# Optimization experiments

Measured on AMD Instinct MI355X. Metric: run time of the kernel, lower is better.

Reference implementation:

```python
import jax, jax.numpy as jnp
import numpy as np

N = 4096
F_IN = 256
F_OUT = 64
H = 4
ALPHA = 0.2  # leaky_relu negative slope
NEG_BIG = -9e15


def setup_inputs() -> dict:
    key = jax.random.key(0)
    k1, k2, k3, k4 = jax.random.split(key, 4)
    x = jax.random.normal(k1, (N, F_IN), dtype=jnp.float32)
    adj = jax.random.randint(k2, (N, N), 0, 2, dtype=jnp.int32)
    # xavier-uniform-like init for params
    limW = float(np.sqrt(6.0 / (F_IN + F_OUT)))
    W = jax.random.uniform(k3, (H, F_IN, F_OUT), jnp.float32, -limW, limW)
    lima = float(np.sqrt(6.0 / (2 * F_OUT + 1)))
    a = jax.random.uniform(k4, (H, 2 * F_OUT, 1), jnp.float32, -lima, lima)
    return {"x": x, "adj": adj, "W": W, "a": a}


def reference(x, adj, W, a):
    # Wh[h,n,o] = x @ W[h]
    Wh = jnp.einsum('nf,hfo->hno', x, W)
    # split attention vector: e[h,i,j] = leaky_relu(a1.Wh_i + a2.Wh_j)
    a1 = a[:, :F_OUT, 0]   # [H, F_OUT]
    a2 = a[:, F_OUT:, 0]   # [H, F_OUT]
    s1 = jnp.einsum('hno,ho->hn', Wh, a1)  # [H, N]
    s2 = jnp.einsum('hno,ho->hn', Wh, a2)  # [H, N]
    e = jax.nn.leaky_relu(s1[:, :, None] + s2[:, None, :], ALPHA)  # [H, N, N]
    e = jnp.where(adj[None, :, :] > 0, e, NEG_BIG)
    att = jax.nn.softmax(e, axis=-1)
    # dropout=0 (eval-mode reference)
    h_prime = jnp.einsum('hij,hjo->hio', att, Wh)  # [H, N, F_OUT]
    # concat heads -> [N, H*F_OUT]
    return jnp.transpose(h_prime, (1, 0, 2)).reshape(N, H * F_OUT)
```

## Files before the change

### kernel.cpp

```cpp
#include <hip/hip_runtime.h>

#define NN 4096
#define FIN 256
#define FOUT 64
#define NH 4

using f32x4 = __attribute__((ext_vector_type(4))) float;
using s16x8 = __attribute__((ext_vector_type(8))) short;
typedef unsigned long long u64;

__device__ __forceinline__ unsigned short f32_to_bf16_rne(float f) {
    unsigned b = __float_as_uint(f);
    b += 0x7FFFu + ((b >> 16) & 1u);
    return (unsigned short)(b >> 16);
}
__device__ __forceinline__ unsigned encf(float f) {
    unsigned b = __float_as_uint(f);
    return (b & 0x80000000u) ? ~b : (b | 0x80000000u);
}
__device__ __forceinline__ float decf(unsigned u) {
    return (u & 0x80000000u) ? __uint_as_float(u & 0x7FFFFFFFu) : __uint_as_float(~u);
}

__global__ __launch_bounds__(256) void k_wh(
    const float* __restrict__ x, const float* __restrict__ W,
    const float* __restrict__ a, short* __restrict__ WhT,
    float* __restrict__ s1, float* __restrict__ s2, unsigned* __restrict__ s2m)
{
    __shared__ unsigned short xs[64 * 256];
    __shared__ unsigned short wt[64 * 256];
    __shared__ float s2red[16];
    const int nb = blockIdx.x, h = blockIdx.y, t = threadIdx.x;
    const int n0 = nb * 64;
    {
        const float4* xg = reinterpret_cast<const float4*>(x + (size_t)n0 * FIN);
        for (int k = t; k < 64 * FIN / 4; k += 256) {
            float4 v = xg[k];
            int row = k >> 6, fq = k & 63;
            u64 pk = (u64)f32_to_bf16_rne(v.x) | ((u64)f32_to_bf16_rne(v.y) << 16)
                   | ((u64)f32_to_bf16_rne(v.z) << 32) | ((u64)f32_to_bf16_rne(v.w) << 48);
            int byte = (row * 512 + fq * 8) ^ ((row & 7) << 4);
            *(u64*)((char*)xs + byte) = pk;
        }
        const float* Wg = W + (size_t)h * FIN * FOUT;
        for (int k = t; k < FIN * FOUT; k += 256) {
            int f = k >> 6, o = k & 63;
            unsigned short wv = f32_to_bf16_rne(Wg[k]);
            int byte = (o * 512 + f * 2) ^ ((o & 7) << 4);
            *(unsigned short*)((char*)wt + byte) = wv;
        }
    }
    __syncthreads();
    const int lane = t & 63, wv_ = t >> 6;
    const int rowA = lane & 15;
    const int kq = (lane >> 4) * 8;
    const int i0 = wv_ * 16;
    f32x4 acc[4];
    #pragma unroll
    for (int c = 0; c < 4; ++c) acc[c] = (f32x4){0.f, 0.f, 0.f, 0.f};
    const int arow = i0 + rowA;
    #pragma unroll
    for (int kb = 0; kb < FIN; kb += 32) {
        int ab = (arow * 512 + (kb + kq) * 2) ^ ((arow & 7) << 4);
        s16x8 af = *(const s16x8*)((char*)xs + ab);
        #pragma unroll
        for (int c = 0; c < 4; ++c) {
            int col = c * 16 + rowA;
            int bb = (col * 512 + (kb + kq) * 2) ^ ((col & 7) << 4);
            s16x8 bf = *(const s16x8*)((char*)wt + bb);
            acc[c] = __builtin_amdgcn_mfma_f32_16x16x32_bf16(af, bf, acc[c], 0, 0, 0);
        }
    }
    const int q0 = (lane >> 4) * 4;
    const float L2E = 1.4426950408889634f;
    float v1acc[4] = {0.f, 0.f, 0.f, 0.f}, v2acc[4] = {0.f, 0.f, 0.f, 0.f};
    #pragma unroll
    for (int c = 0; c < 4; ++c) {
        int col = c * 16 + rowA;
        float a1v = a[h * (2 * FOUT) + col];
        float a2v = a[h * (2 * FOUT) + FOUT + col];
        short* wp = WhT + ((size_t)(h * FOUT + col)) * NN + n0 + i0 + q0;
        alignas(8) unsigned short tmp[4];
        #pragma unroll
        for (int q = 0; q < 4; ++q) {
            float v = acc[c][q];
            tmp[q] = f32_to_bf16_rne(v);
            v1acc[q] = fmaf(v, a1v, v1acc[q]);
            v2acc[q] = fmaf(v, a2v, v2acc[q]);
        }
        __builtin_memcpy(wp, tmp, 8);
    }
    float wmax = -3.0e38f;
    #pragma unroll
    for (int q = 0; q < 4; ++q) {
        float v1 = v1acc[q] * L2E, v2 = v2acc[q] * L2E;
        #pragma unroll
        for (int d = 1; d < 16; d <<= 1) {
            v1 += __shfl_xor(v1, d, 64);
            v2 += __shfl_xor(v2, d, 64);
        }
        if (rowA == 0) {
            int n = n0 + i0 + q0 + q;
            s1[h * NN + n] = v1;
            s2[h * NN + n] = v2;
            wmax = fmaxf(wmax, v2);
        }
    }
    if (rowA == 0) s2red[wv_ * 4 + (lane >> 4)] = wmax;
    __syncthreads();
    if (t == 0) {
        float m = s2red[0];
        #pragma unroll
        for (int i = 1; i < 16; ++i) m = fmaxf(m, s2red[i]);
        atomicMax(&s2m[h], encf(m));
    }
}

__global__ __launch_bounds__(256) void k_pack(const int* __restrict__ adj,
                                              u64* __restrict__ packed,
                                              unsigned* __restrict__ s2m)
{
    const int t = threadIdx.x;
    if (blockIdx.x == 0 && t < NH) s2m[t] = 0u;
    const int lane = t & 63;
    const int jc = t >> 6;
    const int row = blockIdx.x;
    const int g = lane >> 4;
    const int li = lane & 15;
    const int* ap = adj + (size_t)row * NN + jc * 1024 + lane * 4;
    int4 v0 = *(const int4*)(ap);
    int4 v1 = *(const int4*)(ap + 256);
    int4 v2 = *(const int4*)(ap + 512);
    int4 v3 = *(const int4*)(ap + 768);
    u64 words[4];
    int4 vv[4] = {v0, v1, v2, v3};
    #pragma unroll
    for (int k = 0; k < 4; ++k) {
        unsigned b = (vv[k].x != 0 ? 1u : 0u) | (vv[k].y != 0 ? 2u : 0u)
                   | (vv[k].z != 0 ? 4u : 0u) | (vv[k].w != 0 ? 8u : 0u);
        u64 field = (u64)b << (4 * li);
        field |= __shfl_xor(field, 1, 64);
        field |= __shfl_xor(field, 2, 64);
        field |= __shfl_xor(field, 4, 64);
        field |= __shfl_xor(field, 8, 64);
        words[k] = field;
    }
    if (li == 0) {
        #pragma unroll
        for (int k = 0; k < 4; ++k)
            packed[(size_t)(jc * 16 + 4 * k + g) * NN + row] = words[k];
    }
}

__global__ __launch_bounds__(1024, 4) void k_attn(
    const u64* __restrict__ packed, const short* __restrict__ WhT,
    const float* __restrict__ s1, const unsigned* __restrict__ s2m,
    const float* __restrict__ s2, float* __restrict__ out)
{
    __shared__ __align__(16) char smraw[16 * 1040 * 4];
    const int t = threadIdx.x;
    const int lane = t & 63;
    const int wid = t >> 6;
    const int rg = wid >> 2;
    const int jq = wid & 3;
    const int ib64 = blockIdx.x;
    const int h = blockIdx.y;
    const int row16 = lane & 15;
    const int kbase = (lane >> 4) * 8;
    const int irow = ib64 * 64 + rg * 16 + row16;

    const float s1v = s1[h * NN + irow];
    const float s2mv = decf(s2m[h]);
    const float ttv = s1v + s2mv;
    const float M = fmaxf(ttv, 0.2f * ttv);
    const float c1v = s1v - M;
    const float c2v = fmaf(0.2f, s1v, -M);

    f32x4 acc[4], acc_l;
    #pragma unroll
    for (int c = 0; c < 4; ++c) acc[c] = (f32x4){0.f, 0.f, 0.f, 0.f};
    acc_l = (f32x4){0.f, 0.f, 0.f, 0.f};
    s16x8 ones;
    #pragma unroll
    for (int i = 0; i < 8; ++i) ones[i] = (short)0x3F80;

    const float* s2q = s2 + h * NN + kbase;
    const u64*   mb  = packed + irow;

    const int gt = rg * 64 + lane;
    const int so = gt >> 3;
    const int sj = (gt & 7) * 8;
    const short* wsrc = WhT + (size_t)h * FOUT * NN;
    char* btb = smraw + jq * 16384;
    const int wb0 = (so * 128 + sj * 2) ^ ((so & 7) << 4);
    const int wb1 = ((so + 32) * 128 + sj * 2) ^ ((so & 7) << 4);

    int rd[4][2];
    #pragma unroll
    for (int c = 0; c < 4; ++c) {
        int o = c * 16 + row16;
        #pragma unroll
        for (int hf = 0; hf < 2; ++hf)
            rd[c][hf] = (o * 128 + (hf * 32 + kbase) * 2) ^ ((o & 7) << 4);
    }

    auto mk = [&](float sa, float sb, unsigned bits, int q0) -> unsigned {
        float e0 = fmaxf(c1v + sa, fmaf(0.2f, sa, c2v));
        float e1 = fmaxf(c1v + sb, fmaf(0.2f, sb, c2v));
        float p0 = __builtin_amdgcn_exp2f(e0);
        float p1 = __builtin_amdgcn_exp2f(e1);
        p0 = (bits & (1u << q0)) ? p0 : 0.f;
        p1 = (bits & (2u << q0)) ? p1 : 0.f;
        unsigned pk;
        asm("v_cvt_pk_bf16_f32 %0, %1, %2" : "=v"(pk) : "v"(p0), "v"(p1));
        return pk;
    };

    const int jbase = jq * 1024;
    auto body = [&](int jb, char* btr, char* btw, u64 cm, f32x4 (&cs)[4],
                    u64& nm, f32x4 (&ns)[4]) {
        int jn = jb + 64;
        int jpf = (jn < jbase + 1024) ? jn : jbase;
        s16x8 st0 = *(const s16x8*)(wsrc + (size_t)so * NN + jpf + sj);
        s16x8 st1 = *(const s16x8*)(wsrc + (size_t)(so + 32) * NN + jpf + sj);
        nm = mb[(size_t)(jpf >> 6) * NN];
        ns[0] = *(const f32x4*)(s2q + jpf);
        ns[1] = *(const f32x4*)(s2q + jpf + 4);
        ns[2] = *(const f32x4*)(s2q + jpf + 32);
        ns[3] = *(const f32x4*)(s2q + jpf + 36);
        unsigned ml8 = ((unsigned)cm >> kbase) & 0xFFu;
        unsigned mh8 = ((unsigned)(cm >> 32) >> kbase) & 0xFFu;
        s16x8 A0, A1;
        unsigned* A0u = reinterpret_cast<unsigned*>(&A0);
        unsigned* A1u = reinterpret_cast<unsigned*>(&A1);
        A0u[0] = mk(cs[0][0], cs[0][1], ml8, 0);
        A0u[1] = mk(cs[0][2], cs[0][3], ml8, 2);
        A0u[2] = mk(cs[1][0], cs[1][1], ml8, 4);
        A0u[3] = mk(cs[1][2], cs[1][3], ml8, 6);
        A1u[0] = mk(cs[2][0], cs[2][1], mh8, 0);
        A1u[1] = mk(cs[2][2], cs[2][3], mh8, 2);
        A1u[2] = mk(cs[3][0], cs[3][1], mh8, 4);
        A1u[3] = mk(cs[3][2], cs[3][3], mh8, 6);
        *(s16x8*)(btw + wb0) = st0;
        *(s16x8*)(btw + wb1) = st1;
        s16x8 b00 = *(const s16x8*)(btr + rd[0][0]);
        s16x8 b01 = *(const s16x8*)(btr + rd[0][1]);
        s16x8 b10 = *(const s16x8*)(btr + rd[1][0]);
        s16x8 b11 = *(const s16x8*)(btr + rd[1][1]);
        s16x8 b20 = *(const s16x8*)(btr + rd[2][0]);
        s16x8 b21 = *(const s16x8*)(btr + rd[2][1]);
        s16x8 b30 = *(const s16x8*)(btr + rd[3][0]);
        s16x8 b31 = *(const s16x8*)(btr + rd[3][1]);
        acc_l  = __builtin_amdgcn_mfma_f32_16x16x32_bf16(A0, ones, acc_l, 0, 0, 0);
        acc_l  = __builtin_amdgcn_mfma_f32_16x16x32_bf16(A1, ones, acc_l, 0, 0, 0);
        acc[0] = __builtin_amdgcn_mfma_f32_16x16x32_bf16(A0, b00, acc[0], 0, 0, 0);
        acc[0] = __builtin_amdgcn_mfma_f32_16x16x32_bf16(A1, b01, acc[0], 0, 0, 0);
        acc[1] = __builtin_amdgcn_mfma_f32_16x16x32_bf16(A0, b10, acc[1], 0, 0, 0);
        acc[1] = __builtin_amdgcn_mfma_f32_16x16x32_bf16(A1, b11, acc[1], 0, 0, 0);
        acc[2] = __builtin_amdgcn_mfma_f32_16x16x32_bf16(A0, b20, acc[2], 0, 0, 0);
        acc[2] = __builtin_amdgcn_mfma_f32_16x16x32_bf16(A1, b21, acc[2], 0, 0, 0);
        acc[3] = __builtin_amdgcn_mfma_f32_16x16x32_bf16(A0, b30, acc[3], 0, 0, 0);
        acc[3] = __builtin_amdgcn_mfma_f32_16x16x32_bf16(A1, b31, acc[3], 0, 0, 0);
    };

    u64 m0, m1;
    f32x4 sv0[4], sv1[4];
    int jb = jbase;
    {
        s16x8 st0 = *(const s16x8*)(wsrc + (size_t)so * NN + jb + sj);
        s16x8 st1 = *(const s16x8*)(wsrc + (size_t)(so + 32) * NN + jb + sj);
        *(s16x8*)(btb + wb0) = st0;
        *(s16x8*)(btb + wb1) = st1;
        m0 = mb[(size_t)(jb >> 6) * NN];
        sv0[0] = *(const f32x4*)(s2q + jb);
        sv0[1] = *(const f32x4*)(s2q + jb + 4);
        sv0[2] = *(const f32x4*)(s2q + jb + 32);
        sv0[3] = *(const f32x4*)(s2q + jb + 36);
    }
    __syncthreads();
    #pragma unroll 1
    for (int it = 0; it < 8; ++it) {
        body(jb, btb, btb + 8192, m0, sv0, m1, sv1);
        __syncthreads();
        body(jb + 64, btb + 8192, btb, m1, sv1, m0, sv0);
        __syncthreads();
        jb += 128;
    }

    float* mw = (float*)smraw + wid * 1040;
    #pragma unroll
    for (int c = 0; c < 4; ++c) {
        #pragma unroll
        for (int q = 0; q < 4; ++q) {
            int r = (lane >> 4) * 4 + q;
            int o = c * 16 + row16;
            mw[r * 64 + o] = acc[c][q];
        }
    }
    if (row16 == 0) {
        #pragma unroll
        for (int q = 0; q < 4; ++q) mw[1024 + (lane >> 4) * 4 + q] = acc_l[q];
    }
    __syncthreads();
    if (jq == 0) {
        const float* p0 = (float*)smraw + (rg * 4 + 0) * 1040;
        const float* p1 = (float*)smraw + (rg * 4 + 1) * 1040;
        const float* p2 = (float*)smraw + (rg * 4 + 2) * 1040;
        const float* p3 = (float*)smraw + (rg * 4 + 3) * 1040;
        #pragma unroll
        for (int k = 0; k < 16; ++k) {
            int idx = k * 64 + lane;
            int r = idx >> 6;
            float v = p0[idx] + p1[idx] + p2[idx] + p3[idx];
            float l = p0[1024 + r] + p1[1024 + r] + p2[1024 + r] + p3[1024 + r];
            int n = ib64 * 64 + rg * 16 + r;
            out[(size_t)n * (NH * FOUT) + h * FOUT + (idx & 63)] = v / l;
        }
    }
}

extern "C" void kernel_launch(void* const* d_in, const int* in_sizes, int n_in,
                              void* d_out, int out_size, void* d_ws, size_t ws_size,
                              hipStream_t stream) {
    (void)in_sizes; (void)n_in; (void)out_size; (void)ws_size;
    const float* x  = (const float*)d_in[0];
    const int*  adj = (const int*)d_in[1];
    const float* W  = (const float*)d_in[2];
    const float* a  = (const float*)d_in[3];
    float* out = (float*)d_out;
    char* ws = (char*)d_ws;

    size_t off = 0;
    short* WhT    = (short*)(ws + off); off += (size_t)NH * FOUT * NN * 2;
    float* s1     = (float*)(ws + off); off += (size_t)NH * NN * 4;
    float* s2     = (float*)(ws + off); off += (size_t)NH * NN * 4;
    unsigned* s2m = (unsigned*)(ws + off); off += 256;
    u64* packed   = (u64*)(ws + off); off += (size_t)(NN / 64) * NN * 8;

    k_pack<<<4096, 256, 0, stream>>>(adj, packed, s2m);
    k_wh<<<dim3(64, 4), 256, 0, stream>>>(x, W, a, WhT, s1, s2, s2m);
    k_attn<<<dim3(64, NH), 1024, 0, stream>>>(packed, WhT, s1, s2m, s2, out);
}
```

Baseline: 62.40 us.

## Merge adjacency packing and Wh projection into one launch, drop atomic max

Combines the adjacency bit-packing kernel and the Wh/score kernel into a single launch, with block IDs above 256 doing packing and the rest doing projection. The global s2 max now comes from per-block maxima written to a small buffer and reduced by a wave shuffle inside the attention kernel, so the float-encoded atomicMax and its zero-init are gone. This saves one kernel launch and lets the two independent prep stages run concurrently. The cost is a heterogeneous grid where the 256 heavy projection blocks may become the tail, plus a small extra reduction at the start of every attention wave.

```diff
diff --git a/kernel.cpp b/kernel.cpp
--- a/kernel.cpp
+++ b/kernel.cpp
@@ -14,23 +14,52 @@
     b += 0x7FFFu + ((b >> 16) & 1u);
     return (unsigned short)(b >> 16);
 }
-__device__ __forceinline__ unsigned encf(float f) {
-    unsigned b = __float_as_uint(f);
-    return (b & 0x80000000u) ? ~b : (b | 0x80000000u);
-}
-__device__ __forceinline__ float decf(unsigned u) {
-    return (u & 0x80000000u) ? __uint_as_float(u & 0x7FFFFFFFu) : __uint_as_float(~u);
-}
-
-__global__ __launch_bounds__(256) void k_wh(
+
+__global__ __launch_bounds__(256) void k_prep(
     const float* __restrict__ x, const float* __restrict__ W,
-    const float* __restrict__ a, short* __restrict__ WhT,
-    float* __restrict__ s1, float* __restrict__ s2, unsigned* __restrict__ s2m)
+    const float* __restrict__ a, const int* __restrict__ adj,
+    short* __restrict__ WhT, float* __restrict__ s1, float* __restrict__ s2,
+    float* __restrict__ blockmax, u64* __restrict__ packed)
 {
     __shared__ unsigned short xs[64 * 256];
     __shared__ unsigned short wt[64 * 256];
     __shared__ float s2red[16];
-    const int nb = blockIdx.x, h = blockIdx.y, t = threadIdx.x;
+    const int bx = blockIdx.x;
+    const int t = threadIdx.x;
+
+    if (bx >= 256) {
+        const int lane = t & 63;
+        const int jc = t >> 6;
+        const int row = bx - 256;
+        const int g = lane >> 4;
+        const int li = lane & 15;
+        const int* ap = adj + (size_t)row * NN + jc * 1024 + lane * 4;
+        int4 v0 = *(const int4*)(ap);
+        int4 v1 = *(const int4*)(ap + 256);
+        int4 v2 = *(const int4*)(ap + 512);
+        int4 v3 = *(const int4*)(ap + 768);
+        u64 words[4];
+        int4 vv[4] = {v0, v1, v2, v3};
+        #pragma unroll
+        for (int k = 0; k < 4; ++k) {
+            unsigned b = (vv[k].x != 0 ? 1u : 0u) | (vv[k].y != 0 ? 2u : 0u)
+                       | (vv[k].z != 0 ? 4u : 0u) | (vv[k].w != 0 ? 8u : 0u);
+            u64 field = (u64)b << (4 * li);
+            field |= __shfl_xor(field, 1, 64);
+            field |= __shfl_xor(field, 2, 64);
+            field |= __shfl_xor(field, 4, 64);
+            field |= __shfl_xor(field, 8, 64);
+            words[k] = field;
+        }
+        if (li == 0) {
+            #pragma unroll
+            for (int k = 0; k < 4; ++k)
+                packed[(size_t)(jc * 16 + 4 * k + g) * NN + row] = words[k];
+        }
+        return;
+    }
+
+    const int nb = bx & 63, h = bx >> 6;
     const int n0 = nb * 64;
     {
         const float4* xg = reinterpret_cast<const float4*>(x + (size_t)n0 * FIN);
@@ -112,49 +141,13 @@
         float m = s2red[0];
         #pragma unroll
         for (int i = 1; i < 16; ++i) m = fmaxf(m, s2red[i]);
-        atomicMax(&s2m[h], encf(m));
-    }
-}
-
-__global__ __launch_bounds__(256) void k_pack(const int* __restrict__ adj,
-                                              u64* __restrict__ packed,
-                                              unsigned* __restrict__ s2m)
-{
-    const int t = threadIdx.x;
-    if (blockIdx.x == 0 && t < NH) s2m[t] = 0u;
-    const int lane = t & 63;
-    const int jc = t >> 6;
-    const int row = blockIdx.x;
-    const int g = lane >> 4;
-    const int li = lane & 15;
-    const int* ap = adj + (size_t)row * NN + jc * 1024 + lane * 4;
-    int4 v0 = *(const int4*)(ap);
-    int4 v1 = *(const int4*)(ap + 256);
-    int4 v2 = *(const int4*)(ap + 512);
-    int4 v3 = *(const int4*)(ap + 768);
-    u64 words[4];
-    int4 vv[4] = {v0, v1, v2, v3};
-    #pragma unroll
-    for (int k = 0; k < 4; ++k) {
-        unsigned b = (vv[k].x != 0 ? 1u : 0u) | (vv[k].y != 0 ? 2u : 0u)
-                   | (vv[k].z != 0 ? 4u : 0u) | (vv[k].w != 0 ? 8u : 0u);
-        u64 field = (u64)b << (4 * li);
-        field |= __shfl_xor(field, 1, 64);
-        field |= __shfl_xor(field, 2, 64);
-        field |= __shfl_xor(field, 4, 64);
-        field |= __shfl_xor(field, 8, 64);
-        words[k] = field;
-    }
-    if (li == 0) {
-        #pragma unroll
-        for (int k = 0; k < 4; ++k)
-            packed[(size_t)(jc * 16 + 4 * k + g) * NN + row] = words[k];
+        blockmax[h * 64 + nb] = m;
     }
 }
 
 __global__ __launch_bounds__(1024, 4) void k_attn(
     const u64* __restrict__ packed, const short* __restrict__ WhT,
-    const float* __restrict__ s1, const unsigned* __restrict__ s2m,
+    const float* __restrict__ s1, const float* __restrict__ blockmax,
     const float* __restrict__ s2, float* __restrict__ out)
 {
     __shared__ __align__(16) char smraw[16 * 1040 * 4];
@@ -169,9 +162,11 @@
     const int kbase = (lane >> 4) * 8;
     const int irow = ib64 * 64 + rg * 16 + row16;
 
+    float bm = blockmax[h * 64 + lane];
+    #pragma unroll
+    for (int d = 32; d >= 1; d >>= 1) bm = fmaxf(bm, __shfl_xor(bm, d, 64));
     const float s1v = s1[h * NN + irow];
-    const float s2mv = decf(s2m[h]);
-    const float ttv = s1v + s2mv;
+    const float ttv = s1v + bm;
     const float M = fmaxf(ttv, 0.2f * ttv);
     const float c1v = s1v - M;
     const float c2v = fmaf(0.2f, s1v, -M);
@@ -331,13 +326,12 @@
     char* ws = (char*)d_ws;
 
     size_t off = 0;
-    short* WhT    = (short*)(ws + off); off += (size_t)NH * FOUT * NN * 2;
-    float* s1     = (float*)(ws + off); off += (size_t)NH * NN * 4;
-    float* s2     = (float*)(ws + off); off += (size_t)NH * NN * 4;
-    unsigned* s2m = (unsigned*)(ws + off); off += 256;
-    u64* packed   = (u64*)(ws + off); off += (size_t)(NN / 64) * NN * 8;
-
-    k_pack<<<4096, 256, 0, stream>>>(adj, packed, s2m);
-    k_wh<<<dim3(64, 4), 256, 0, stream>>>(x, W, a, WhT, s1, s2, s2m);
-    k_attn<<<dim3(64, NH), 1024, 0, stream>>>(packed, WhT, s1, s2m, s2, out);
+    short* WhT      = (short*)(ws + off); off += (size_t)NH * FOUT * NN * 2;
+    float* s1       = (float*)(ws + off); off += (size_t)NH * NN * 4;
+    float* s2       = (float*)(ws + off); off += (size_t)NH * NN * 4;
+    float* blockmax = (float*)(ws + off); off += (size_t)NH * 64 * 4;
+    u64* packed     = (u64*)(ws + off); off += (size_t)(NN / 64) * NN * 8;
+
+    k_prep<<<4352, 256, 0, stream>>>(x, W, a, adj, WhT, s1, s2, blockmax, packed);
+    k_attn<<<dim3(64, NH), 1024, 0, stream>>>(packed, WhT, s1, blockmax, s2, out);
 }
```

Measured after the change: 52.95 us. 15.2% less time.
